# Kernel tuning notes

Measured on AMD Instinct MI355X. Metric: run time of the kernel, lower is better.

Reference implementation:

```python
import jax, jax.numpy as jnp
import numpy as np

DIM = 384
NUM_HEADS = 8
HEAD_DIM = DIM // NUM_HEADS
SCALE = HEAD_DIM ** -0.5
MLP_HIDDEN = int(DIM * 4.0)
EPS = 1e-6


def setup_inputs() -> dict:
    key = jax.random.key(0)
    ks = jax.random.split(key, 8)
    s = 0.02
    return {
        "x": jax.random.normal(ks[0], (2, DIM, 8, 16, 16), dtype=jnp.float32),
        "g1": jnp.ones((DIM,), jnp.float32),
        "b1": jnp.zeros((DIM,), jnp.float32),
        "Wqkv": jax.random.normal(ks[1], (DIM, 3 * DIM), jnp.float32) * s,  # no bias (qkv_bias=False)
        "Wo": jax.random.normal(ks[2], (DIM, DIM), jnp.float32) * s,
        "bo": jnp.zeros((DIM,), jnp.float32),
        "g2": jnp.ones((DIM,), jnp.float32),
        "b2": jnp.zeros((DIM,), jnp.float32),
        "W1": jax.random.normal(ks[3], (DIM, MLP_HIDDEN), jnp.float32) * s,
        "b1m": jnp.zeros((MLP_HIDDEN,), jnp.float32),
        "W2": jax.random.normal(ks[4], (MLP_HIDDEN, DIM), jnp.float32) * s,
        "b2m": jnp.zeros((DIM,), jnp.float32),
    }


def _layernorm(x, g, b):
    mu = jnp.mean(x, axis=-1, keepdims=True)
    var = jnp.mean(jnp.square(x - mu), axis=-1, keepdims=True)
    return (x - mu) * jax.lax.rsqrt(var + EPS) * g + b


def _attention(h, Wqkv, Wo, bo):
    B, N, C = h.shape
    qkv = h @ Wqkv  # [B, N, 3C]
    qkv = qkv.reshape(B, N, 3, NUM_HEADS, HEAD_DIM).transpose(2, 0, 3, 1, 4)
    q, k, v = qkv[0], qkv[1], qkv[2]  # each [B, H, N, d]
    att = jax.nn.softmax(jnp.einsum('bhxd,bhyd->bhxy', q, k) * SCALE, axis=-1)
    out = jnp.einsum('bhxy,bhyd->bhxd', att, v)  # [B, H, N, d]
    out = out.transpose(0, 2, 1, 3).reshape(B, N, C)
    return out @ Wo + bo


def reference(x, g1, b1, Wqkv, Wo, bo, g2, b2, W1, b1m, W2, b2m):
    B, C, D, H, W = x.shape
    h = x.transpose(0, 2, 3, 4, 1).reshape(B, D * H * W, C)  # b (d h w) c
    h = h + _attention(_layernorm(h, g1, b1), Wqkv, Wo, bo)
    m = _layernorm(h, g2, b2)
    m = jax.nn.gelu(m @ W1 + b1m, approximate=False) @ W2 + b2m
    h = h + m
    return h.reshape(B, D, H, W, C).transpose(0, 4, 1, 2, 3)
```

## Files before the change

### kernel.cpp

```cpp
#include <hip/hip_runtime.h>
#include <hip/hip_bf16.h>
#include <math.h>

#define DIM    384
#define NHEAD  8
#define HDIM   48
#define NTOK   2048
#define BATCH  2
#define TOKS   (BATCH * NTOK)
#define HIDDEN 1536

typedef __bf16 bf16x8 __attribute__((ext_vector_type(8)));
typedef float  f32x4  __attribute__((ext_vector_type(4)));
typedef unsigned short u16;

union bfu { __hip_bfloat16 h; u16 u; };

__device__ __forceinline__ void load_lds16(const void* g, void* l) {
    __builtin_amdgcn_global_load_lds(
        (const __attribute__((address_space(1))) void*)g,
        (__attribute__((address_space(3))) void*)l, 16, 0, 0);
}

__global__ __launch_bounds__(256) void prep(
    const float* __restrict__ Wqkv, const float* __restrict__ Wo,
    const float* __restrict__ W1,   const float* __restrict__ W2,
    __hip_bfloat16* __restrict__ WqkvT, __hip_bfloat16* __restrict__ WoT,
    __hip_bfloat16* __restrict__ W1T,   __hip_bfloat16* __restrict__ W2T,
    const float* __restrict__ x, const float* __restrict__ g,
    const float* __restrict__ bta,
    float* __restrict__ hOut, __hip_bfloat16* __restrict__ y) {
    __shared__ __align__(16) char smem[384 * 33 * 4];
    int id = blockIdx.x;
    int tid = threadIdx.x;
    if (id < 1728) {
        float (*t)[33] = (float(*)[33])smem;
        const float* src; __hip_bfloat16* dst; int R, C;
        if (id < 432)       { src = Wqkv; dst = WqkvT; R = 384;  C = 1152; }
        else if (id < 576)  { id -= 432;  src = Wo;    dst = WoT;  R = 384;  C = 384; }
        else if (id < 1152) { id -= 576;  src = W1;    dst = W1T;  R = 384;  C = 1536; }
        else                { id -= 1152; src = W2;    dst = W2T;  R = 1536; C = 384; }
        int tc = C / 32;
        int i0 = (id / tc) * 32, j0 = (id % tc) * 32;
        int tx = tid & 31, ty = tid >> 5;
#pragma unroll
        for (int k = 0; k < 32; k += 8)
            t[ty + k][tx] = src[(size_t)(i0 + ty + k) * C + j0 + tx];
        __syncthreads();
#pragma unroll
        for (int k = 0; k < 32; k += 8)
            dst[(size_t)(j0 + ty + k) * R + i0 + tx] = __float2bfloat16(t[tx][ty + k]);
    } else {
        float* t = (float*)smem;
        int id2 = id - 1728;
        int n0 = (id2 & 63) * 32, b = id2 >> 6;
        const float* xb = x + (size_t)b * DIM * NTOK;
        for (int idx = tid; idx < 384 * 32; idx += 256) {
            int c = idx >> 5, n = idx & 31;
            t[c * 33 + n] = xb[(size_t)c * NTOK + n0 + n];
        }
        __syncthreads();
        int wid = tid >> 6, lane = tid & 63;
#pragma unroll
        for (int it = 0; it < 8; ++it) {
            int tl = it * 4 + wid;
            float v[6];
            float s = 0.f;
#pragma unroll
            for (int i = 0; i < 6; ++i) { v[i] = t[(lane + 64 * i) * 33 + tl]; s += v[i]; }
#pragma unroll
            for (int o = 32; o; o >>= 1) s += __shfl_xor(s, o, 64);
            float mu = s * (1.f / DIM);
            float s2 = 0.f;
#pragma unroll
            for (int i = 0; i < 6; ++i) { float d = v[i] - mu; s2 += d * d; }
#pragma unroll
            for (int o = 32; o; o >>= 1) s2 += __shfl_xor(s2, o, 64);
            float r = rsqrtf(s2 * (1.f / DIM) + 1e-6f);
            size_t tok = (size_t)b * NTOK + n0 + tl;
#pragma unroll
            for (int i = 0; i < 6; ++i) {
                int c = lane + 64 * i;
                hOut[tok * DIM + c] = v[i];
                y[tok * DIM + c] = __float2bfloat16((v[i] - mu) * r * g[c] + bta[c]);
            }
        }
    }
}

__global__ __launch_bounds__(256) void ln_kernel(const float* __restrict__ x,
                                                 const float* __restrict__ g,
                                                 const float* __restrict__ bta,
                                                 __hip_bfloat16* __restrict__ y) {
    int wid = threadIdx.x >> 6, lane = threadIdx.x & 63;
    int tok = blockIdx.x * 4 + wid;
    const float* xr = x + (size_t)tok * DIM;
    float v[6];
    float s = 0.f;
#pragma unroll
    for (int i = 0; i < 6; ++i) { v[i] = xr[lane + 64 * i]; s += v[i]; }
#pragma unroll
    for (int o = 32; o; o >>= 1) s += __shfl_xor(s, o, 64);
    float mu = s * (1.f / DIM);
    float s2 = 0.f;
#pragma unroll
    for (int i = 0; i < 6; ++i) { float d = v[i] - mu; s2 += d * d; }
#pragma unroll
    for (int o = 32; o; o >>= 1) s2 += __shfl_xor(s2, o, 64);
    float r = rsqrtf(s2 * (1.f / DIM) + 1e-6f);
    __hip_bfloat16* yr = y + (size_t)tok * DIM;
#pragma unroll
    for (int i = 0; i < 6; ++i) {
        int c = lane + 64 * i;
        yr[c] = __float2bfloat16((v[i] - mu) * r * g[c] + bta[c]);
    }
}

template<bool GELU, bool BF16OUT, bool TRANSOUT, bool QKV>
__global__ __launch_bounds__(256) void gemm_mfma(
    const __hip_bfloat16* __restrict__ A,
    const __hip_bfloat16* __restrict__ BT,
    const float* __restrict__ bias,
    const float* __restrict__ res,
    void* __restrict__ Cout,
    int M, int N, int K,
    __hip_bfloat16* __restrict__ vtout) {
    __shared__ __align__(16) u16 As[4][64 * 32];
    __shared__ __align__(16) u16 Bs[4][64 * 32];
    int bm = blockIdx.y * 64, bn = blockIdx.x * 64;
    int tid = threadIdx.x;
    int w = tid >> 6, l = tid & 63;
    int m0 = (w >> 1) * 32, n0 = (w & 1) * 32;
    int lm = l & 15, ksel = l >> 4;

    int row = tid >> 2, c16 = tid & 3;
    const __hip_bfloat16* ga = A  + (size_t)(bm + row) * K + c16 * 8;
    const __hip_bfloat16* gb = BT + (size_t)(bn + row) * K + c16 * 8;

    f32x4 acc[2][2] = {};
    for (int k0 = 0; k0 < K; k0 += 128) {
#pragma unroll
        for (int kk = 0; kk < 4; ++kk) {
            load_lds16(ga + k0 + kk * 32, &As[kk][tid * 8]);
            load_lds16(gb + k0 + kk * 32, &Bs[kk][tid * 8]);
        }
        __syncthreads();
#pragma unroll
        for (int kk = 0; kk < 4; ++kk) {
            bf16x8 af0 = *(const bf16x8*)&As[kk][(m0 +      lm) * 32 + ksel * 8];
            bf16x8 af1 = *(const bf16x8*)&As[kk][(m0 + 16 + lm) * 32 + ksel * 8];
            bf16x8 bf0 = *(const bf16x8*)&Bs[kk][(n0 +      lm) * 32 + ksel * 8];
            bf16x8 bf1 = *(const bf16x8*)&Bs[kk][(n0 + 16 + lm) * 32 + ksel * 8];
            acc[0][0] = __builtin_amdgcn_mfma_f32_16x16x32_bf16(af0, bf0, acc[0][0], 0, 0, 0);
            acc[0][1] = __builtin_amdgcn_mfma_f32_16x16x32_bf16(af0, bf1, acc[0][1], 0, 0, 0);
            acc[1][0] = __builtin_amdgcn_mfma_f32_16x16x32_bf16(af1, bf0, acc[1][0], 0, 0, 0);
            acc[1][1] = __builtin_amdgcn_mfma_f32_16x16x32_bf16(af1, bf1, acc[1][1], 0, 0, 0);
        }
        __syncthreads();
    }

    if constexpr (TRANSOUT) {
        __shared__ float ct[64 * 65];
#pragma unroll
        for (int i = 0; i < 2; ++i)
#pragma unroll
            for (int j = 0; j < 2; ++j)
#pragma unroll
                for (int r = 0; r < 4; ++r) {
                    int ml = m0 + i * 16 + ksel * 4 + r;
                    int cl = n0 + j * 16 + lm;
                    float v = acc[i][j][r];
                    if (bias) v += bias[bn + cl];
                    if (res)  v += res[(size_t)(bm + ml) * N + bn + cl];
                    ct[ml * 65 + cl] = v;
                }
        __syncthreads();
        int bb = bm >> 11, nb = bm & (NTOK - 1);
        float* outp = (float*)Cout + (size_t)bb * DIM * NTOK + nb;
#pragma unroll
        for (int cl = w; cl < 64; cl += 4)
            outp[(size_t)(bn + cl) * NTOK + l] = ct[l * 65 + cl];
    } else {
#pragma unroll
        for (int i = 0; i < 2; ++i)
#pragma unroll
            for (int j = 0; j < 2; ++j)
#pragma unroll
                for (int r = 0; r < 4; ++r) {
                    int rg = bm + m0 + i * 16 + ksel * 4 + r;
                    int cg = bn + n0 + j * 16 + lm;
                    float v = acc[i][j][r];
                    if (bias) v += bias[cg];
                    if (GELU) v = 0.5f * v * (1.f + erff(v * 0.7071067811865475f));
                    if (res)  v += res[(size_t)rg * N + cg];
                    if constexpr (QKV) {
                        if (cg < 768) {
                            ((__hip_bfloat16*)Cout)[(size_t)rg * 1152 + cg] = __float2bfloat16(v);
                        } else {
                            int c = cg - 768, hh = c / 48, dd = c - hh * 48;
                            int bb = rg >> 11, n = rg & (NTOK - 1);
                            int kk = n & 127;
                            int pos = ((kk >> 6) << 6) + ((kk & 15) << 2) + ((kk >> 4) & 3);
                            vtout[((size_t)(bb * NHEAD + hh) * 48 + dd) * 2048
                                  + (n & ~127) + pos] = __float2bfloat16(v);
                        }
                    } else if constexpr (BF16OUT) {
                        ((__hip_bfloat16*)Cout)[(size_t)rg * N + cg] = __float2bfloat16(v);
                    } else {
                        ((float*)Cout)[(size_t)rg * N + cg] = v;
                    }
                }
    }
}

#define ATK 128
#define PSTR 136
__global__ __launch_bounds__(512, 6) void attn_mfma(
    const u16* __restrict__ qkv,
    const u16* __restrict__ vt,
    __hip_bfloat16* __restrict__ outp) {
    __shared__ __align__(16) u16 PQ[64 * PSTR];
    __shared__ __align__(16) u16 Ks[128 * 72];
    __shared__ __align__(16) u16 Vs[48 * PSTR];
    const int q0 = blockIdx.x * 64;
    const int h = blockIdx.y, b = blockIdx.z;
    const int tid = threadIdx.x;
    const int w = tid >> 6, l = tid & 63, lm = l & 15, quad = l >> 4;
    const int qc = w >> 1, kh = w & 1;

    for (int idx = tid; idx < 128; idx += 512) {
        int r = idx >> 1, c = idx & 1;
        *(uint4*)&PQ[r * 72 + 48 + c * 8] = uint4{0, 0, 0, 0};
    }
    for (int idx = tid; idx < 256; idx += 512) {
        int r = idx >> 1, c = idx & 1;
        *(uint4*)&Ks[r * 72 + 48 + c * 8] = uint4{0, 0, 0, 0};
    }
    const u16* qbase = qkv + (size_t)(b * NTOK + q0) * 1152 + h * 48;
    for (int idx = tid; idx < 384; idx += 512) {
        int r = idx / 6, c = idx % 6;
        *(uint4*)&PQ[r * 72 + c * 8] = *(const uint4*)(qbase + (size_t)r * 1152 + c * 8);
    }
    __syncthreads();

    bf16x8 aq0 = *(const bf16x8*)&PQ[(qc * 16 + lm) * 72 +  0 + quad * 8];
    bf16x8 aq1 = *(const bf16x8*)&PQ[(qc * 16 + lm) * 72 + 32 + quad * 8];

    float l_i[4] = {0.f, 0.f, 0.f, 0.f};
    f32x4 o_acc[3] = {};

    const u16* kbase = qkv + (size_t)(b * NTOK) * 1152 + 384 + h * 48;
    const u16* vbase = vt + (size_t)(b * NHEAD + h) * 48 * 2048;
    const float sc2 = 0.14433756729740643f * 1.4426950408889634f;

    for (int kt = 0; kt < NTOK / ATK; ++kt) {
        __syncthreads();
#pragma unroll
        for (int idx = tid; idx < 768; idx += 512) {
            int r = idx / 6, c = idx % 6;
            *(uint4*)&Ks[r * 72 + c * 8] =
                *(const uint4*)(kbase + (size_t)(kt * ATK + r) * 1152 + c * 8);
        }
#pragma unroll
        for (int idx = tid; idx < 768; idx += 512) {
            int d = idx >> 4, c = idx & 15;
            *(uint4*)&Vs[d * PSTR + c * 8] =
                *(const uint4*)(vbase + (size_t)d * 2048 + kt * ATK + c * 8);
        }
        __syncthreads();

        f32x4 s[4];
#pragma unroll
        for (int ntp = 0; ntp < 4; ++ntp) {
            int nt = kh * 4 + ntp;
            bf16x8 kf0 = *(const bf16x8*)&Ks[(nt * 16 + lm) * 72 +  0 + quad * 8];
            bf16x8 kf1 = *(const bf16x8*)&Ks[(nt * 16 + lm) * 72 + 32 + quad * 8];
            f32x4 t = {};
            t = __builtin_amdgcn_mfma_f32_16x16x32_bf16(aq0, kf0, t, 0, 0, 0);
            t = __builtin_amdgcn_mfma_f32_16x16x32_bf16(aq1, kf1, t, 0, 0, 0);
            s[ntp] = t;
        }

#pragma unroll
        for (int r = 0; r < 4; ++r) {
            u16 pr[4];
#pragma unroll
            for (int ntp = 0; ntp < 4; ++ntp) {
                float p = exp2f(s[ntp][r] * sc2);
                l_i[r] += p;
                bfu cv; cv.h = __float2bfloat16(p);
                pr[ntp] = cv.u;
            }
            *(uint2*)&PQ[(qc * 16 + quad * 4 + r) * PSTR + kh * 64 + lm * 4] =
                *(const uint2*)pr;
        }

#pragma unroll
        for (int ksp = 0; ksp < 2; ++ksp) {
            int ks = kh * 2 + ksp;
            bf16x8 pf = *(const bf16x8*)&PQ[(qc * 16 + lm) * PSTR + ks * 32 + quad * 8];
#pragma unroll
            for (int nt = 0; nt < 3; ++nt) {
                bf16x8 vf = *(const bf16x8*)&Vs[(nt * 16 + lm) * PSTR + ks * 32 + quad * 8];
                o_acc[nt] = __builtin_amdgcn_mfma_f32_16x16x32_bf16(pf, vf, o_acc[nt], 0, 0, 0);
            }
        }
    }

    __syncthreads();
    float* red = (float*)Ks;
    if (kh == 1) {
        f32x4* base = (f32x4*)&red[(qc * 64 + l) * 16];
        base[0] = o_acc[0]; base[1] = o_acc[1]; base[2] = o_acc[2];
        f32x4 lv; lv[0] = l_i[0]; lv[1] = l_i[1]; lv[2] = l_i[2]; lv[3] = l_i[3];
        base[3] = lv;
    }
    __syncthreads();
    if (kh == 0) {
        f32x4* base = (f32x4*)&red[(qc * 64 + l) * 16];
        o_acc[0] += base[0]; o_acc[1] += base[1]; o_acc[2] += base[2];
        f32x4 lv = base[3];
#pragma unroll
        for (int r = 0; r < 4; ++r) {
            float lsum = l_i[r] + lv[r];
#pragma unroll
            for (int o = 8; o; o >>= 1) lsum += __shfl_xor(lsum, o, 64);
            float inv = 1.f / lsum;
#pragma unroll
            for (int nt = 0; nt < 3; ++nt)
                outp[(size_t)(b * NTOK + q0 + qc * 16 + quad * 4 + r) * DIM
                     + h * 48 + nt * 16 + lm]
                    = __float2bfloat16(o_acc[nt][r] * inv);
        }
    }
}

extern "C" void kernel_launch(void* const* d_in, const int* in_sizes, int n_in,
                              void* d_out, int out_size, void* d_ws, size_t ws_size,
                              hipStream_t stream) {
    const float* x    = (const float*)d_in[0];
    const float* g1   = (const float*)d_in[1];
    const float* b1   = (const float*)d_in[2];
    const float* Wqkv = (const float*)d_in[3];
    const float* Wo   = (const float*)d_in[4];
    const float* bo   = (const float*)d_in[5];
    const float* g2   = (const float*)d_in[6];
    const float* b2   = (const float*)d_in[7];
    const float* W1   = (const float*)d_in[8];
    const float* b1m  = (const float*)d_in[9];
    const float* W2   = (const float*)d_in[10];
    const float* b2m  = (const float*)d_in[11];
    float* out = (float*)d_out;

    char* p = (char*)d_ws;
    float* bufH = (float*)p;                       p += (size_t)TOKS * DIM * 4;
    char* qkvp = p;
    __hip_bfloat16* bufQKVb = (__hip_bfloat16*)p;  p += (size_t)TOKS * 3 * DIM * 2;
    __hip_bfloat16* bufVT   = (__hip_bfloat16*)p;  p += (size_t)TOKS * DIM * 2;
    __hip_bfloat16* bufNb   = (__hip_bfloat16*)p;  p += (size_t)TOKS * DIM * 2;
    __hip_bfloat16* bufAb   = (__hip_bfloat16*)p;  p += (size_t)TOKS * DIM * 2;
    __hip_bfloat16* WqkvT   = (__hip_bfloat16*)p;  p += (size_t)3 * DIM * DIM * 2;
    __hip_bfloat16* WoT     = (__hip_bfloat16*)p;  p += (size_t)DIM * DIM * 2;
    __hip_bfloat16* W1T     = (__hip_bfloat16*)p;  p += (size_t)HIDDEN * DIM * 2;
    __hip_bfloat16* W2T     = (__hip_bfloat16*)p;  p += (size_t)DIM * HIDDEN * 2;
    __hip_bfloat16* bufHIDb = (__hip_bfloat16*)qkvp;

    prep<<<1728 + 128, 256, 0, stream>>>(Wqkv, Wo, W1, W2, WqkvT, WoT, W1T, W2T,
                                         x, g1, b1, bufH, bufNb);
    gemm_mfma<false, true, false, true><<<dim3(3 * DIM / 64, TOKS / 64), 256, 0, stream>>>(
        bufNb, WqkvT, nullptr, nullptr, bufQKVb, TOKS, 3 * DIM, DIM, bufVT);
    attn_mfma<<<dim3(NTOK / 64, NHEAD, BATCH), 512, 0, stream>>>(
        (const u16*)bufQKVb, (const u16*)bufVT, bufAb);
    gemm_mfma<false, false, false, false><<<dim3(DIM / 64, TOKS / 64), 256, 0, stream>>>(
        bufAb, WoT, bo, bufH, bufH, TOKS, DIM, DIM, nullptr);
    ln_kernel<<<TOKS / 4, 256, 0, stream>>>(bufH, g2, b2, bufNb);
    gemm_mfma<true, true, false, false><<<dim3(HIDDEN / 64, TOKS / 64), 256, 0, stream>>>(
        bufNb, W1T, b1m, nullptr, bufHIDb, TOKS, HIDDEN, DIM, nullptr);
    gemm_mfma<false, false, true, false><<<dim3(DIM / 64, TOKS / 64), 256, 0, stream>>>(
        bufHIDb, W2T, b2m, bufH, out, TOKS, DIM, HIDDEN, nullptr);
}
```

Measured before the change: 198.1 us.

## Split attention waves 2x4 over queries and keys with register-reused K/V fragments

Attention waves are reorganized from 4 query-chunks by 2 key-halves into 2 query-chunks of 32 rows by 4 key-quarters, so each wave reuses its K and V fragments across two 16-row query subtiles. The V-transpose write layout in the QKV GEMM epilogue is changed to match the new 32-key slices. The cross-wave reduction becomes a staged 4-way sum through LDS with extra barriers. The occupancy hint is dropped from launch bounds, which may raise register use.

```diff
diff --git a/kernel.cpp b/kernel.cpp
--- a/kernel.cpp
+++ b/kernel.cpp
@@ -200,7 +200,7 @@
                             int c = cg - 768, hh = c / 48, dd = c - hh * 48;
                             int bb = rg >> 11, n = rg & (NTOK - 1);
                             int kk = n & 127;
-                            int pos = ((kk >> 6) << 6) + ((kk & 15) << 2) + ((kk >> 4) & 3);
+                            int pos = (kk & ~31) + ((kk & 15) << 1) + ((kk >> 4) & 1);
                             vtout[((size_t)(bb * NHEAD + hh) * 48 + dd) * 2048
                                   + (n & ~127) + pos] = __float2bfloat16(v);
                         }
@@ -215,7 +215,7 @@
 
 #define ATK 128
 #define PSTR 136
-__global__ __launch_bounds__(512, 6) void attn_mfma(
+__global__ __launch_bounds__(512) void attn_mfma(
     const u16* __restrict__ qkv,
     const u16* __restrict__ vt,
     __hip_bfloat16* __restrict__ outp) {
@@ -226,7 +226,7 @@
     const int h = blockIdx.y, b = blockIdx.z;
     const int tid = threadIdx.x;
     const int w = tid >> 6, l = tid & 63, lm = l & 15, quad = l >> 4;
-    const int qc = w >> 1, kh = w & 1;
+    const int qc = w >> 2, kh = w & 3;
 
     for (int idx = tid; idx < 128; idx += 512) {
         int r = idx >> 1, c = idx & 1;
@@ -243,11 +243,15 @@
     }
     __syncthreads();
 
-    bf16x8 aq0 = *(const bf16x8*)&PQ[(qc * 16 + lm) * 72 +  0 + quad * 8];
-    bf16x8 aq1 = *(const bf16x8*)&PQ[(qc * 16 + lm) * 72 + 32 + quad * 8];
-
-    float l_i[4] = {0.f, 0.f, 0.f, 0.f};
-    f32x4 o_acc[3] = {};
+    bf16x8 aq[2][2];
+#pragma unroll
+    for (int qsub = 0; qsub < 2; ++qsub) {
+        aq[qsub][0] = *(const bf16x8*)&PQ[(qc * 32 + qsub * 16 + lm) * 72 +  0 + quad * 8];
+        aq[qsub][1] = *(const bf16x8*)&PQ[(qc * 32 + qsub * 16 + lm) * 72 + 32 + quad * 8];
+    }
+
+    float l_i[8] = {};
+    f32x4 o_acc[2][3] = {};
 
     const u16* kbase = qkv + (size_t)(b * NTOK) * 1152 + 384 + h * 48;
     const u16* vbase = vt + (size_t)(b * NHEAD + h) * 48 * 2048;
@@ -269,69 +273,133 @@
         }
         __syncthreads();
 
-        f32x4 s[4];
-#pragma unroll
-        for (int ntp = 0; ntp < 4; ++ntp) {
-            int nt = kh * 4 + ntp;
-            bf16x8 kf0 = *(const bf16x8*)&Ks[(nt * 16 + lm) * 72 +  0 + quad * 8];
-            bf16x8 kf1 = *(const bf16x8*)&Ks[(nt * 16 + lm) * 72 + 32 + quad * 8];
-            f32x4 t = {};
-            t = __builtin_amdgcn_mfma_f32_16x16x32_bf16(aq0, kf0, t, 0, 0, 0);
-            t = __builtin_amdgcn_mfma_f32_16x16x32_bf16(aq1, kf1, t, 0, 0, 0);
-            s[ntp] = t;
-        }
-
-#pragma unroll
-        for (int r = 0; r < 4; ++r) {
-            u16 pr[4];
-#pragma unroll
-            for (int ntp = 0; ntp < 4; ++ntp) {
-                float p = exp2f(s[ntp][r] * sc2);
-                l_i[r] += p;
-                bfu cv; cv.h = __float2bfloat16(p);
-                pr[ntp] = cv.u;
+        f32x4 s[2][2];
+#pragma unroll
+        for (int nt = 0; nt < 2; ++nt) {
+            int krow = (kh * 32 + nt * 16 + lm) * 72;
+            bf16x8 kf0 = *(const bf16x8*)&Ks[krow +  0 + quad * 8];
+            bf16x8 kf1 = *(const bf16x8*)&Ks[krow + 32 + quad * 8];
+#pragma unroll
+            for (int qsub = 0; qsub < 2; ++qsub) {
+                f32x4 t = {};
+                t = __builtin_amdgcn_mfma_f32_16x16x32_bf16(aq[qsub][0], kf0, t, 0, 0, 0);
+                t = __builtin_amdgcn_mfma_f32_16x16x32_bf16(aq[qsub][1], kf1, t, 0, 0, 0);
+                s[qsub][nt] = t;
             }
-            *(uint2*)&PQ[(qc * 16 + quad * 4 + r) * PSTR + kh * 64 + lm * 4] =
-                *(const uint2*)pr;
-        }
-
-#pragma unroll
-        for (int ksp = 0; ksp < 2; ++ksp) {
-            int ks = kh * 2 + ksp;
-            bf16x8 pf = *(const bf16x8*)&PQ[(qc * 16 + lm) * PSTR + ks * 32 + quad * 8];
-#pragma unroll
-            for (int nt = 0; nt < 3; ++nt) {
-                bf16x8 vf = *(const bf16x8*)&Vs[(nt * 16 + lm) * PSTR + ks * 32 + quad * 8];
-                o_acc[nt] = __builtin_amdgcn_mfma_f32_16x16x32_bf16(pf, vf, o_acc[nt], 0, 0, 0);
+        }
+
+#pragma unroll
+        for (int qsub = 0; qsub < 2; ++qsub)
+#pragma unroll
+            for (int r = 0; r < 4; ++r) {
+                float p0 = exp2f(s[qsub][0][r] * sc2);
+                float p1 = exp2f(s[qsub][1][r] * sc2);
+                l_i[qsub * 4 + r] += p0 + p1;
+                bfu c0, c1; c0.h = __float2bfloat16(p0); c1.h = __float2bfloat16(p1);
+                unsigned int packed = (unsigned int)c0.u | ((unsigned int)c1.u << 16);
+                *(unsigned int*)&PQ[(qc * 32 + qsub * 16 + quad * 4 + r) * PSTR
+                                    + kh * 32 + lm * 2] = packed;
             }
-        }
-    }
-
+
+        bf16x8 vf[3];
+#pragma unroll
+        for (int nt = 0; nt < 3; ++nt)
+            vf[nt] = *(const bf16x8*)&Vs[(nt * 16 + lm) * PSTR + kh * 32 + quad * 8];
+#pragma unroll
+        for (int qsub = 0; qsub < 2; ++qsub) {
+            bf16x8 pf = *(const bf16x8*)&PQ[(qc * 32 + qsub * 16 + lm) * PSTR
+                                            + kh * 32 + quad * 8];
+#pragma unroll
+            for (int nt = 0; nt < 3; ++nt)
+                o_acc[qsub][nt] = __builtin_amdgcn_mfma_f32_16x16x32_bf16(
+                    pf, vf[nt], o_acc[qsub][nt], 0, 0, 0);
+        }
+    }
+
+    float* oScr = (float*)Ks;
+    float* lScr = (float*)Vs;
     __syncthreads();
-    float* red = (float*)Ks;
-    if (kh == 1) {
-        f32x4* base = (f32x4*)&red[(qc * 64 + l) * 16];
-        base[0] = o_acc[0]; base[1] = o_acc[1]; base[2] = o_acc[2];
-        f32x4 lv; lv[0] = l_i[0]; lv[1] = l_i[1]; lv[2] = l_i[2]; lv[3] = l_i[3];
-        base[3] = lv;
+    if (kh > 0) {
+        float* lb = &lScr[qc * 1536 + (kh - 1) * 512 + l * 8];
+        *(f32x4*)lb       = *(f32x4*)&l_i[0];
+        *(f32x4*)(lb + 4) = *(f32x4*)&l_i[4];
+        if (qc == 0) {
+            float* ob = &oScr[(kh - 1) * 1536 + l * 24];
+#pragma unroll
+            for (int qsub = 0; qsub < 2; ++qsub)
+#pragma unroll
+                for (int nt = 0; nt < 3; ++nt)
+                    *(f32x4*)(ob + (qsub * 3 + nt) * 4) = o_acc[qsub][nt];
+        }
     }
     __syncthreads();
-    if (kh == 0) {
-        f32x4* base = (f32x4*)&red[(qc * 64 + l) * 16];
-        o_acc[0] += base[0]; o_acc[1] += base[1]; o_acc[2] += base[2];
-        f32x4 lv = base[3];
-#pragma unroll
-        for (int r = 0; r < 4; ++r) {
-            float lsum = l_i[r] + lv[r];
-#pragma unroll
-            for (int o = 8; o; o >>= 1) lsum += __shfl_xor(lsum, o, 64);
-            float inv = 1.f / lsum;
+    if (kh == 0 && qc == 0) {
+#pragma unroll
+        for (int sct = 0; sct < 3; ++sct) {
+            float* ob = &oScr[sct * 1536 + l * 24];
+            float* lb = &lScr[0 * 1536 + sct * 512 + l * 8];
+#pragma unroll
+            for (int qsub = 0; qsub < 2; ++qsub)
+#pragma unroll
+                for (int nt = 0; nt < 3; ++nt)
+                    o_acc[qsub][nt] += *(f32x4*)(ob + (qsub * 3 + nt) * 4);
+            f32x4 la = *(f32x4*)lb, lbv = *(f32x4*)(lb + 4);
+#pragma unroll
+            for (int r = 0; r < 4; ++r) { l_i[r] += la[r]; l_i[4 + r] += lbv[r]; }
+        }
+#pragma unroll
+        for (int qsub = 0; qsub < 2; ++qsub)
+#pragma unroll
+            for (int r = 0; r < 4; ++r) {
+                float lsum = l_i[qsub * 4 + r];
+#pragma unroll
+                for (int o = 8; o; o >>= 1) lsum += __shfl_xor(lsum, o, 64);
+                float inv = 1.f / lsum;
+#pragma unroll
+                for (int nt = 0; nt < 3; ++nt)
+                    outp[(size_t)(b * NTOK + q0 + 0 * 32 + qsub * 16 + quad * 4 + r) * DIM
+                         + h * 48 + nt * 16 + lm]
+                        = __float2bfloat16(o_acc[qsub][nt][r] * inv);
+            }
+    }
+    __syncthreads();
+    if (kh > 0 && qc == 1) {
+        float* ob = &oScr[(kh - 1) * 1536 + l * 24];
+#pragma unroll
+        for (int qsub = 0; qsub < 2; ++qsub)
 #pragma unroll
             for (int nt = 0; nt < 3; ++nt)
-                outp[(size_t)(b * NTOK + q0 + qc * 16 + quad * 4 + r) * DIM
-                     + h * 48 + nt * 16 + lm]
-                    = __float2bfloat16(o_acc[nt][r] * inv);
-        }
+                *(f32x4*)(ob + (qsub * 3 + nt) * 4) = o_acc[qsub][nt];
+    }
+    __syncthreads();
+    if (kh == 0 && qc == 1) {
+#pragma unroll
+        for (int sct = 0; sct < 3; ++sct) {
+            float* ob = &oScr[sct * 1536 + l * 24];
+            float* lb = &lScr[1 * 1536 + sct * 512 + l * 8];
+#pragma unroll
+            for (int qsub = 0; qsub < 2; ++qsub)
+#pragma unroll
+                for (int nt = 0; nt < 3; ++nt)
+                    o_acc[qsub][nt] += *(f32x4*)(ob + (qsub * 3 + nt) * 4);
+            f32x4 la = *(f32x4*)lb, lbv = *(f32x4*)(lb + 4);
+#pragma unroll
+            for (int r = 0; r < 4; ++r) { l_i[r] += la[r]; l_i[4 + r] += lbv[r]; }
+        }
+#pragma unroll
+        for (int qsub = 0; qsub < 2; ++qsub)
+#pragma unroll
+            for (int r = 0; r < 4; ++r) {
+                float lsum = l_i[qsub * 4 + r];
+#pragma unroll
+                for (int o = 8; o; o >>= 1) lsum += __shfl_xor(lsum, o, 64);
+                float inv = 1.f / lsum;
+#pragma unroll
+                for (int nt = 0; nt < 3; ++nt)
+                    outp[(size_t)(b * NTOK + q0 + 1 * 32 + qsub * 16 + quad * 4 + r) * DIM
+                         + h * 48 + nt * 16 + lm]
+                        = __float2bfloat16(o_acc[qsub][nt][r] * inv);
+            }
     }
 }
 
```

Measured after the change: 202.8 us. 2.4% more time.
